# Kernel optimization log

Measured on AMD Instinct MI355X. Metric: run time of the kernel, lower is better.

The kernel has to match this reference:

```python
import jax, jax.numpy as jnp
import numpy as np

FEATURES = 8
POINTS = 3
CLASSES = 128
BATCH = 1024
TEMPERATURE = 0.1


def setup_inputs() -> dict:
    key = jax.random.key(0)
    k1, k2, k3 = jax.random.split(key, 3)
    x = jax.random.normal(k1, (BATCH, FEATURES), dtype=jnp.float32)
    beta = jax.random.uniform(k2, (FEATURES, POINTS), dtype=jnp.float32)
    classifier = jax.random.uniform(
        k3, ((POINTS + 1) ** FEATURES, CLASSES), dtype=jnp.float32)
    return {"x": x, "beta": beta, "classifier": classifier}


def reference(x, beta, classifier):
    # b: sort beta ascending per-feature, negate, cumsum, prepend a zero bin edge
    T = 1.0 / TEMPERATURE
    bneg = jnp.cumsum(-jnp.sort(beta, axis=1), axis=1)            # [F, P]
    b = jnp.concatenate(
        [jnp.zeros((beta.shape[0], 1), beta.dtype), bneg], axis=1)  # [F, P+1]
    w = jnp.arange(1, POINTS + 2, dtype=x.dtype)                  # [P+1]
    # soft one-hot binning per feature: [B, F, P+1]
    logits = (x[:, :, None] * w[None, None, :] + b[None, :, :]) * T
    hot = jax.nn.softmax(logits, axis=-1)
    # iterative outer product over features -> joint leaf histogram [B, (P+1)^F]
    B = x.shape[0]
    leaves = hot[:, 0, :]
    for f in range(1, FEATURES):  # small fixed loop over features
        leaves = (leaves[:, :, None] * hot[:, f, None, :]).reshape(B, -1)
    return leaves @ classifier  # [B, classes]
```

## Files before the change

kernel.cpp:

```cpp
#include <hip/hip_runtime.h>
#include <stdint.h>

typedef unsigned short u16;
typedef __attribute__((ext_vector_type(4))) float f32x4;
typedef __attribute__((ext_vector_type(2))) float f32x2;
typedef __attribute__((ext_vector_type(8))) short s16x8;

#define T_INV 10.0f
#define QEPS 9.5367431640625e-07f

__device__ __forceinline__ u16 f2bf(float f) {
  uint32_t u = __float_as_uint(f);
  uint32_t r = (u + 0x7FFFu + ((u >> 16) & 1u)) >> 16;
  return (u16)r;
}

__device__ __forceinline__ void gload_lds16(const void* g, void* l) {
  __builtin_amdgcn_global_load_lds(
      (const __attribute__((address_space(1))) uint32_t*)(g),
      (__attribute__((address_space(3))) uint32_t*)(l),
      16, 0, 0);
}

__global__ __launch_bounds__(256) void k_prep(
    const float* __restrict__ cls, const float* __restrict__ x,
    const float* __restrict__ beta,
    u16* __restrict__ ct, u16* __restrict__ plo, float* __restrict__ phiT)
{
  const int t = threadIdx.x;
  if (blockIdx.x < 1024) {
    __shared__ float tile[64 * 132];
    const int k0 = blockIdx.x * 64;
#pragma unroll
    for (int it = 0; it < 8; ++it) {
      int e = it * 1024 + t * 4;
      int r = e >> 7;
      int c = e & 127;
      f32x4 v = *(const f32x4*)(cls + (size_t)(k0 + r) * 128 + c);
      *(f32x4*)(tile + r * 132 + c) = v;
    }
    __syncthreads();
    const int c  = t >> 1;
    const int kh = t & 1;
    u16 vals[32];
#pragma unroll
    for (int j = 0; j < 32; ++j)
      vals[j] = f2bf(tile[(kh*32 + j) * 132 + c]);
    u16* dst = ct + ((size_t)(k0 >> 3) + kh * 4) * 1024 + c * 8;
#pragma unroll
    for (int qq = 0; qq < 4; ++qq) {
      s16x8 v;
#pragma unroll
      for (int e2 = 0; e2 < 8; ++e2) v[e2] = (short)vals[qq*8 + e2];
      *(s16x8*)(dst + (size_t)qq * 1024) = v;
    }
  } else {
    const int b = (blockIdx.x - 1024) * 64 + (t >> 2);
    const int q = t & 3;
    float hot[8][4];
#pragma unroll
    for (int f = 0; f < 8; ++f) {
      float b0 = beta[f*3+0], b1 = beta[f*3+1], b2 = beta[f*3+2];
      float s0 = fminf(b0, fminf(b1, b2));
      float s2 = fmaxf(b0, fmaxf(b1, b2));
      float s1 = b0 + b1 + b2 - s0 - s2;
      float bv1 = -s0, bv2 = -(s0 + s1), bv3 = -(s0 + s1 + s2);
      float xf = x[b*8 + f];
      float l0 = (xf * 1.0f       ) * T_INV;
      float l1 = (xf * 2.0f + bv1) * T_INV;
      float l2 = (xf * 3.0f + bv2) * T_INV;
      float l3 = (xf * 4.0f + bv3) * T_INV;
      float mm = fmaxf(fmaxf(l0, l1), fmaxf(l2, l3));
      float e0 = __expf(l0 - mm), e1 = __expf(l1 - mm);
      float e2 = __expf(l2 - mm), e3 = __expf(l3 - mm);
      float inv = 1.0f / (e0 + e1 + e2 + e3);
      hot[f][0] = e0*inv; hot[f][1] = e1*inv; hot[f][2] = e2*inv; hot[f][3] = e3*inv;
    }
    {
      float h23[16];
#pragma unroll
      for (int i2 = 0; i2 < 4; ++i2)
#pragma unroll
        for (int i3 = 0; i3 < 4; ++i3) h23[i2*4+i3] = hot[2][i2] * hot[3][i3];
      float h0q = hot[0][q];
#pragma unroll
      for (int i1 = 0; i1 < 4; ++i1) {
        float c01 = h0q * hot[1][i1];
#pragma unroll
        for (int j = 0; j < 16; ++j)
          phiT[(size_t)(q*64 + i1*16 + j) * 1024 + b] = c01 * h23[j];
      }
    }
    {
      float h67[16];
#pragma unroll
      for (int i6 = 0; i6 < 4; ++i6)
#pragma unroll
        for (int i7 = 0; i7 < 4; ++i7) h67[i6*4+i7] = hot[6][i6] * hot[7][i7];
      float h4q = hot[4][q];
      u16* dst = plo + (size_t)b*256 + q*64;
#pragma unroll
      for (int i5 = 0; i5 < 4; ++i5) {
        float c45 = h4q * hot[5][i5];
#pragma unroll
        for (int j = 0; j < 16; j += 8) {
          s16x8 v;
#pragma unroll
          for (int e = 0; e < 8; ++e) v[e] = (short)f2bf(c45 * h67[j+e]);
          *(s16x8*)(dst + i5*16 + j) = v;
        }
      }
    }
  }
}

__global__ __launch_bounds__(512, 4) void k_main(
    const u16* __restrict__ plo, const float* __restrict__ phiT,
    const u16* __restrict__ ct, u16* __restrict__ pws)
{
  __shared__ __align__(16) u16 As[32768];
  __shared__ __align__(16) u16 Bb[2][4096];

  const int wg  = blockIdx.x;
  const int xcd = wg & 7;
  const int idx = wg >> 3;
  const int hig = xcd * 8 + (idx >> 3);
  const int m   = idx & 7;

  const int t    = threadIdx.x;
  const int l    = t & 63;
  const int w    = t >> 6;
  const int lrow = l & 15;
  const int kg   = l >> 4;
  const int rbase = (w >> 2) * 64;
  const int cbase = (w & 3) * 32;

  const u16* ploM = plo + (size_t)m * 128 * 256;

#pragma unroll
  for (int i = 0; i < 8; ++i) {
    int row = t >> 2;
    int g   = ((t & 3) - ((t >> 3) & 3)) & 3;
    gload_lds16(ploM + (size_t)row * 256 + i * 32 + g * 8, &As[i * 4096 + t * 8]);
  }

  int aoff[4], boff[2];
#pragma unroll
  for (int mt = 0; mt < 4; ++mt) {
    int row = rbase + mt * 16 + lrow;
    aoff[mt] = row * 32 + (((kg + ((row >> 1) & 3)) & 3)) * 8;
  }
#pragma unroll
  for (int nt = 0; nt < 2; ++nt) {
    int c = cbase + nt * 16 + lrow;
    boff[nt] = c * 32 + (((kg + ((c >> 1) & 3)) & 3)) * 8;
  }

  const int bc = t & 127;
  const int bg = t >> 7;
  const u16* bsrc = ct + (size_t)hig * 131072 + (size_t)bc * 8
                       + (size_t)bg * 1024;
  const int sB = (bg + ((bc >> 1) & 3)) & 3;

  s16x8 bregE, bregO;
  bregE = *(const s16x8*)(bsrc + 0 * 4096);
  bregO = *(const s16x8*)(bsrc + 1 * 4096);
  *(s16x8*)(&Bb[0][bc * 32 + sB * 8]) = bregE;
  __syncthreads();

  f32x4 qprev[4];
  {
    const float* p0 = phiT + (size_t)(hig * 4) * 1024 + m * 128;
#pragma unroll
    for (int mt = 0; mt < 4; ++mt) {
      f32x4 q = *(const f32x4*)(p0 + rbase + mt * 16 + kg * 4);
#pragma unroll
      for (int r = 0; r < 4; ++r) qprev[mt][r] = fmaxf(q[r], QEPS);
    }
  }

  f32x4 acc[4][2];
#pragma unroll
  for (int i = 0; i < 4; ++i)
#pragma unroll
    for (int j = 0; j < 2; ++j) acc[i][j] = (f32x4)0.0f;

  s16x8 afrP[4];
#pragma unroll
  for (int mt = 0; mt < 4; ++mt)
    afrP[mt] = *(const s16x8*)(&As[aoff[mt]]);

#pragma unroll 1
  for (int h = 0; h < 4; ++h) {
#pragma unroll
    for (int ks = 0; ks < 8; ++ks) {
      const int tt = h * 8 + ks;
      if (h < 3 || ks < 6) {
        const u16* p = bsrc + (size_t)(tt + 2) * 4096;
        if (ks & 1) bregO = *(const s16x8*)p;
        else        bregE = *(const s16x8*)p;
      }
      s16x8 bfr[2];
#pragma unroll
      for (int nt = 0; nt < 2; ++nt)
        bfr[nt] = *(const s16x8*)(&Bb[ks & 1][boff[nt]]);
      __builtin_amdgcn_s_setprio(1);
#pragma unroll
      for (int mt = 0; mt < 4; ++mt)
#pragma unroll
        for (int nt = 0; nt < 2; ++nt)
          acc[mt][nt] = __builtin_amdgcn_mfma_f32_16x16x32_bf16(
              afrP[mt], bfr[nt], acc[mt][nt], 0, 0, 0);
      __builtin_amdgcn_s_setprio(0);
      {
        const int nks = (ks + 1) & 7;
#pragma unroll
        for (int mt = 0; mt < 4; ++mt)
          afrP[mt] = *(const s16x8*)(&As[nks * 4096 + aoff[mt]]);
      }
      if (h < 3 || ks < 7) {
        u16* d = &Bb[(ks + 1) & 1][bc * 32 + sB * 8];
        *(s16x8*)d = (ks & 1) ? bregE : bregO;
      }
      asm volatile("s_waitcnt lgkmcnt(0)" ::: "memory");
      __builtin_amdgcn_sched_barrier(0);
      __builtin_amdgcn_s_barrier();
      __builtin_amdgcn_sched_barrier(0);
    }
    if (h < 3) {
      const float* pn = phiT + (size_t)(hig * 4 + h + 1) * 1024 + m * 128;
#pragma unroll
      for (int mt = 0; mt < 4; ++mt) {
        f32x4 qn = *(const f32x4*)(pn + rbase + mt * 16 + kg * 4);
        f32x4 ratio;
#pragma unroll
        for (int r = 0; r < 4; ++r) {
          float q = fmaxf(qn[r], QEPS);
          ratio[r] = qprev[mt][r] * __builtin_amdgcn_rcpf(q);
          qprev[mt][r] = q;
        }
#pragma unroll
        for (int nt = 0; nt < 2; ++nt)
#pragma unroll
          for (int r = 0; r < 4; ++r)
            acc[mt][nt][r] *= ratio[r];
      }
    }
  }

  __syncthreads();
  {
    u16* ob = As;
#pragma unroll
    for (int mt = 0; mt < 4; ++mt)
#pragma unroll
      for (int r = 0; r < 4; ++r) {
        int row = rbase + mt * 16 + kg * 4 + r;
#pragma unroll
        for (int nt = 0; nt < 2; ++nt) {
          int col = cbase + nt * 16 + lrow;
          ob[row * 136 + col] = f2bf(acc[mt][nt][r] * qprev[mt][r]);
        }
      }
    __syncthreads();
    const int row = t >> 2;
    const int q4  = t & 3;
    const u16* srcp = ob + row * 136 + q4 * 32;
    u16* gdst = pws + ((size_t)hig * 1024 + (size_t)m * 128) * 128
                    + row * 128 + q4 * 32;
#pragma unroll
    for (int i = 0; i < 4; ++i)
      *(s16x8*)(gdst + i * 8) = *(const s16x8*)(srcp + i * 8);
  }
}

__global__ __launch_bounds__(256) void k_reduce(
    const u16* __restrict__ p, float* __restrict__ out)
{
  const int g = blockIdx.x * 256 + threadIdx.x;
  const u16* src = p + (size_t)g * 2;
  float a0 = 0.0f, a1 = 0.0f;
#pragma unroll 8
  for (int hig = 0; hig < 64; ++hig) {
    uint32_t v = *(const uint32_t*)(src + (size_t)hig * 131072);
    a0 += __uint_as_float((v & 0xFFFFu) << 16);
    a1 += __uint_as_float(v & 0xFFFF0000u);
  }
  f32x2 o; o.x = a0; o.y = a1;
  *(f32x2*)(out + (size_t)g * 2) = o;
}

extern "C" void kernel_launch(void* const* d_in, const int* in_sizes, int n_in,
                              void* d_out, int out_size, void* d_ws, size_t ws_size,
                              hipStream_t stream)
{
  const float* x    = (const float*)d_in[0];
  const float* beta = (const float*)d_in[1];
  const float* cls  = (const float*)d_in[2];
  float* out = (float*)d_out;

  char* ws = (char*)d_ws;
  u16*   ct   = (u16*)ws;
  u16*   plo  = (u16*)(ws + (16u << 20));
  float* phiT = (float*)(ws + (16u << 20) + 524288);
  u16*   pws  = (u16*)(ws + (16u << 20) + 524288 + 1048576);

  k_prep<<<1040, 256, 0, stream>>>(cls, x, beta, ct, plo, phiT);
  k_main<<<512, 512, 0, stream>>>(plo, phiT, ct, pws);
  k_reduce<<<256, 256, 0, stream>>>(pws, out);
}
```

Measured before the change: 46.72 us.

## Double k_main threads, stage B via direct-to-LDS loads with 4-deep ring

```diff
diff --git a/kernel.cpp b/kernel.cpp
--- a/kernel.cpp
+++ b/kernel.cpp
@@ -114,12 +114,12 @@
   }
 }
 
-__global__ __launch_bounds__(512, 4) void k_main(
+__global__ __launch_bounds__(1024) void k_main(
     const u16* __restrict__ plo, const float* __restrict__ phiT,
     const u16* __restrict__ ct, u16* __restrict__ pws)
 {
   __shared__ __align__(16) u16 As[32768];
-  __shared__ __align__(16) u16 Bb[2][4096];
+  __shared__ __align__(16) u16 Bb[4][4096];
 
   const int wg  = blockIdx.x;
   const int xcd = wg & 7;
@@ -132,118 +132,118 @@
   const int w    = t >> 6;
   const int lrow = l & 15;
   const int kg   = l >> 4;
-  const int rbase = (w >> 2) * 64;
+  const int rbase = (w >> 2) * 32;
   const int cbase = (w & 3) * 32;
 
   const u16* ploM = plo + (size_t)m * 128 * 256;
 
 #pragma unroll
-  for (int i = 0; i < 8; ++i) {
-    int row = t >> 2;
-    int g   = ((t & 3) - ((t >> 3) & 3)) & 3;
-    gload_lds16(ploM + (size_t)row * 256 + i * 32 + g * 8, &As[i * 4096 + t * 8]);
-  }
-
-  int aoff[4], boff[2];
-#pragma unroll
-  for (int mt = 0; mt < 4; ++mt) {
+  for (int i = 0; i < 4; ++i) {
+    int ks   = i * 2 + (t >> 9);
+    int idx2 = t & 511;
+    int row  = idx2 >> 2;
+    int g    = ((idx2 & 3) - ((row >> 1) & 3)) & 3;
+    gload_lds16(ploM + (size_t)row * 256 + ks * 32 + g * 8,
+                &As[ks * 4096 + idx2 * 8]);
+  }
+
+  const int stg  = (t < 512);
+  const int scol = (t >> 2) & 127;
+  const int sgr  = ((t & 3) - ((scol >> 1) & 3)) & 3;
+  auto stageB = [&](int kc) {
+    if (stg)
+      gload_lds16(ct + (((size_t)(hig * 128 + kc * 4 + sgr)) << 10) + scol * 8,
+                  &Bb[kc & 3][(t & 511) * 8]);
+  };
+
+  stageB(0); stageB(1); stageB(2);
+  asm volatile("s_waitcnt vmcnt(0)" ::: "memory");
+  __builtin_amdgcn_sched_barrier(0);
+  __builtin_amdgcn_s_barrier();
+  __builtin_amdgcn_sched_barrier(0);
+
+  s16x8 areg[2][8];
+#pragma unroll
+  for (int mt = 0; mt < 2; ++mt) {
     int row = rbase + mt * 16 + lrow;
-    aoff[mt] = row * 32 + (((kg + ((row >> 1) & 3)) & 3)) * 8;
-  }
+    int off = row * 32 + (((kg + ((row >> 1) & 3)) & 3)) * 8;
+#pragma unroll
+    for (int ks = 0; ks < 8; ++ks)
+      areg[mt][ks] = *(const s16x8*)(&As[ks * 4096 + off]);
+  }
+
+  int boff[2];
 #pragma unroll
   for (int nt = 0; nt < 2; ++nt) {
     int c = cbase + nt * 16 + lrow;
     boff[nt] = c * 32 + (((kg + ((c >> 1) & 3)) & 3)) * 8;
   }
 
-  const int bc = t & 127;
-  const int bg = t >> 7;
-  const u16* bsrc = ct + (size_t)hig * 131072 + (size_t)bc * 8
-                       + (size_t)bg * 1024;
-  const int sB = (bg + ((bc >> 1) & 3)) & 3;
-
-  s16x8 bregE, bregO;
-  bregE = *(const s16x8*)(bsrc + 0 * 4096);
-  bregO = *(const s16x8*)(bsrc + 1 * 4096);
-  *(s16x8*)(&Bb[0][bc * 32 + sB * 8]) = bregE;
-  __syncthreads();
-
-  f32x4 qprev[4];
+  f32x4 qprev[2];
   {
     const float* p0 = phiT + (size_t)(hig * 4) * 1024 + m * 128;
 #pragma unroll
-    for (int mt = 0; mt < 4; ++mt) {
+    for (int mt = 0; mt < 2; ++mt) {
       f32x4 q = *(const f32x4*)(p0 + rbase + mt * 16 + kg * 4);
 #pragma unroll
       for (int r = 0; r < 4; ++r) qprev[mt][r] = fmaxf(q[r], QEPS);
     }
   }
 
-  f32x4 acc[4][2];
-#pragma unroll
-  for (int i = 0; i < 4; ++i)
+  f32x4 acc[2][2];
+#pragma unroll
+  for (int i = 0; i < 2; ++i)
 #pragma unroll
     for (int j = 0; j < 2; ++j) acc[i][j] = (f32x4)0.0f;
-
-  s16x8 afrP[4];
-#pragma unroll
-  for (int mt = 0; mt < 4; ++mt)
-    afrP[mt] = *(const s16x8*)(&As[aoff[mt]]);
 
 #pragma unroll 1
   for (int h = 0; h < 4; ++h) {
 #pragma unroll
     for (int ks = 0; ks < 8; ++ks) {
-      const int tt = h * 8 + ks;
-      if (h < 3 || ks < 6) {
-        const u16* p = bsrc + (size_t)(tt + 2) * 4096;
-        if (ks & 1) bregO = *(const s16x8*)p;
-        else        bregE = *(const s16x8*)p;
-      }
+      const int kc = h * 8 + ks;
+      if (h < 3 || ks < 5) stageB(kc + 3);
       s16x8 bfr[2];
 #pragma unroll
       for (int nt = 0; nt < 2; ++nt)
-        bfr[nt] = *(const s16x8*)(&Bb[ks & 1][boff[nt]]);
+        bfr[nt] = *(const s16x8*)(&Bb[ks & 3][boff[nt]]);
       __builtin_amdgcn_s_setprio(1);
 #pragma unroll
-      for (int mt = 0; mt < 4; ++mt)
+      for (int mt = 0; mt < 2; ++mt)
 #pragma unroll
         for (int nt = 0; nt < 2; ++nt)
           acc[mt][nt] = __builtin_amdgcn_mfma_f32_16x16x32_bf16(
-              afrP[mt], bfr[nt], acc[mt][nt], 0, 0, 0);
+              areg[mt][ks], bfr[nt], acc[mt][nt], 0, 0, 0);
       __builtin_amdgcn_s_setprio(0);
-      {
-        const int nks = (ks + 1) & 7;
-#pragma unroll
-        for (int mt = 0; mt < 4; ++mt)
-          afrP[mt] = *(const s16x8*)(&As[nks * 4096 + aoff[mt]]);
-      }
-      if (h < 3 || ks < 7) {
-        u16* d = &Bb[(ks + 1) & 1][bc * 32 + sB * 8];
-        *(s16x8*)d = (ks & 1) ? bregE : bregO;
-      }
-      asm volatile("s_waitcnt lgkmcnt(0)" ::: "memory");
-      __builtin_amdgcn_sched_barrier(0);
-      __builtin_amdgcn_s_barrier();
-      __builtin_amdgcn_sched_barrier(0);
-    }
-    if (h < 3) {
-      const float* pn = phiT + (size_t)(hig * 4 + h + 1) * 1024 + m * 128;
-#pragma unroll
-      for (int mt = 0; mt < 4; ++mt) {
-        f32x4 qn = *(const f32x4*)(pn + rbase + mt * 16 + kg * 4);
-        f32x4 ratio;
-#pragma unroll
-        for (int r = 0; r < 4; ++r) {
-          float q = fmaxf(qn[r], QEPS);
-          ratio[r] = qprev[mt][r] * __builtin_amdgcn_rcpf(q);
-          qprev[mt][r] = q;
+      if (ks == 7 && h < 3) {
+        const float* pn = phiT + (size_t)(hig * 4 + h + 1) * 1024 + m * 128;
+#pragma unroll
+        for (int mt = 0; mt < 2; ++mt) {
+          f32x4 qn = *(const f32x4*)(pn + rbase + mt * 16 + kg * 4);
+          f32x4 ratio;
+#pragma unroll
+          for (int r = 0; r < 4; ++r) {
+            float q = fmaxf(qn[r], QEPS);
+            ratio[r] = qprev[mt][r] * __builtin_amdgcn_rcpf(q);
+            qprev[mt][r] = q;
+          }
+#pragma unroll
+          for (int nt = 0; nt < 2; ++nt)
+#pragma unroll
+            for (int r = 0; r < 4; ++r)
+              acc[mt][nt][r] *= ratio[r];
         }
-#pragma unroll
-        for (int nt = 0; nt < 2; ++nt)
-#pragma unroll
-          for (int r = 0; r < 4; ++r)
-            acc[mt][nt][r] *= ratio[r];
+      }
+      if (kc <= 28) {
+        asm volatile("s_waitcnt vmcnt(2)" ::: "memory");
+      } else if (kc == 29) {
+        asm volatile("s_waitcnt vmcnt(1)" ::: "memory");
+      } else if (kc == 30) {
+        asm volatile("s_waitcnt vmcnt(0)" ::: "memory");
+      }
+      if (kc < 31) {
+        __builtin_amdgcn_sched_barrier(0);
+        __builtin_amdgcn_s_barrier();
+        __builtin_amdgcn_sched_barrier(0);
       }
     }
   }
@@ -252,7 +252,7 @@
   {
     u16* ob = As;
 #pragma unroll
-    for (int mt = 0; mt < 4; ++mt)
+    for (int mt = 0; mt < 2; ++mt)
 #pragma unroll
       for (int r = 0; r < 4; ++r) {
         int row = rbase + mt * 16 + kg * 4 + r;
@@ -263,14 +263,13 @@
         }
       }
     __syncthreads();
-    const int row = t >> 2;
-    const int q4  = t & 3;
-    const u16* srcp = ob + row * 136 + q4 * 32;
-    u16* gdst = pws + ((size_t)hig * 1024 + (size_t)m * 128) * 128
-                    + row * 128 + q4 * 32;
-#pragma unroll
-    for (int i = 0; i < 4; ++i)
-      *(s16x8*)(gdst + i * 8) = *(const s16x8*)(srcp + i * 8);
+    const int row = t >> 3;
+    const int seg = t & 7;
+    const u16* srcp = ob + row * 136 + seg * 16;
+    u16* gdst = pws + ((size_t)hig * 1024 + (size_t)m * 128 + row) * 128
+                    + seg * 16;
+    *(s16x8*)(gdst)     = *(const s16x8*)(srcp);
+    *(s16x8*)(gdst + 8) = *(const s16x8*)(srcp + 8);
   }
 }
 
@@ -306,6 +305,6 @@
   u16*   pws  = (u16*)(ws + (16u << 20) + 524288 + 1048576);
 
   k_prep<<<1040, 256, 0, stream>>>(cls, x, beta, ct, plo, phiT);
-  k_main<<<512, 512, 0, stream>>>(plo, phiT, ct, pws);
+  k_main<<<512, 1024, 0, stream>>>(plo, phiT, ct, pws);
   k_reduce<<<256, 256, 0, stream>>>(pws, out);
 }
```

After: 50.62 us. 1.08x slower.

## Stage B tiles via direct global-to-LDS loads with coarser double buffering

Applied to the files above, without the earlier changes.

```diff
diff --git a/kernel.cpp b/kernel.cpp
--- a/kernel.cpp
+++ b/kernel.cpp
@@ -114,12 +114,12 @@
   }
 }
 
-__global__ __launch_bounds__(512, 4) void k_main(
+__global__ __launch_bounds__(512) void k_main(
     const u16* __restrict__ plo, const float* __restrict__ phiT,
     const u16* __restrict__ ct, u16* __restrict__ pws)
 {
   __shared__ __align__(16) u16 As[32768];
-  __shared__ __align__(16) u16 Bb[2][4096];
+  __shared__ __align__(16) u16 Bp[2][16384];
 
   const int wg  = blockIdx.x;
   const int xcd = wg & 7;
@@ -140,9 +140,20 @@
 #pragma unroll
   for (int i = 0; i < 8; ++i) {
     int row = t >> 2;
-    int g   = ((t & 3) - ((t >> 3) & 3)) & 3;
+    int g   = ((t & 3) - ((row >> 1) & 3)) & 3;
     gload_lds16(ploM + (size_t)row * 256 + i * 32 + g * 8, &As[i * 4096 + t * 8]);
   }
+
+  const int scol = t >> 2;
+  const int ssl  = t & 3;
+  const int sgr  = (ssl - ((scol >> 1) & 3)) & 3;
+  auto stageB = [&](int p, int buf) {
+#pragma unroll
+    for (int s = 0; s < 4; ++s)
+      gload_lds16(ct + (((size_t)(hig * 128 + p * 16 + s * 4 + sgr)) << 10)
+                     + scol * 8,
+                  &Bp[buf][s * 4096 + t * 8]);
+  };
 
   int aoff[4], boff[2];
 #pragma unroll
@@ -156,17 +167,11 @@
     boff[nt] = c * 32 + (((kg + ((c >> 1) & 3)) & 3)) * 8;
   }
 
-  const int bc = t & 127;
-  const int bg = t >> 7;
-  const u16* bsrc = ct + (size_t)hig * 131072 + (size_t)bc * 8
-                       + (size_t)bg * 1024;
-  const int sB = (bg + ((bc >> 1) & 3)) & 3;
-
-  s16x8 bregE, bregO;
-  bregE = *(const s16x8*)(bsrc + 0 * 4096);
-  bregO = *(const s16x8*)(bsrc + 1 * 4096);
-  *(s16x8*)(&Bb[0][bc * 32 + sB * 8]) = bregE;
-  __syncthreads();
+  stageB(0, 0);
+  asm volatile("s_waitcnt vmcnt(0)" ::: "memory");
+  __builtin_amdgcn_sched_barrier(0);
+  __builtin_amdgcn_s_barrier();
+  __builtin_amdgcn_sched_barrier(0);
 
   f32x4 qprev[4];
   {
@@ -185,50 +190,31 @@
 #pragma unroll
     for (int j = 0; j < 2; ++j) acc[i][j] = (f32x4)0.0f;
 
-  s16x8 afrP[4];
-#pragma unroll
-  for (int mt = 0; mt < 4; ++mt)
-    afrP[mt] = *(const s16x8*)(&As[aoff[mt]]);
-
 #pragma unroll 1
-  for (int h = 0; h < 4; ++h) {
-#pragma unroll
-    for (int ks = 0; ks < 8; ++ks) {
-      const int tt = h * 8 + ks;
-      if (h < 3 || ks < 6) {
-        const u16* p = bsrc + (size_t)(tt + 2) * 4096;
-        if (ks & 1) bregO = *(const s16x8*)p;
-        else        bregE = *(const s16x8*)p;
-      }
-      s16x8 bfr[2];
+  for (int p = 0; p < 8; ++p) {
+    if (p < 7) stageB(p + 1, (p + 1) & 1);
+    const u16* B  = &Bp[p & 1][0];
+    const int ksb = (p & 1) * 4;
+#pragma unroll
+    for (int s = 0; s < 4; ++s) {
+      s16x8 afr[4], bfr[2];
+#pragma unroll
+      for (int mt = 0; mt < 4; ++mt)
+        afr[mt] = *(const s16x8*)(&As[(ksb + s) * 4096 + aoff[mt]]);
 #pragma unroll
       for (int nt = 0; nt < 2; ++nt)
-        bfr[nt] = *(const s16x8*)(&Bb[ks & 1][boff[nt]]);
+        bfr[nt] = *(const s16x8*)(B + s * 4096 + boff[nt]);
       __builtin_amdgcn_s_setprio(1);
 #pragma unroll
       for (int mt = 0; mt < 4; ++mt)
 #pragma unroll
         for (int nt = 0; nt < 2; ++nt)
           acc[mt][nt] = __builtin_amdgcn_mfma_f32_16x16x32_bf16(
-              afrP[mt], bfr[nt], acc[mt][nt], 0, 0, 0);
+              afr[mt], bfr[nt], acc[mt][nt], 0, 0, 0);
       __builtin_amdgcn_s_setprio(0);
-      {
-        const int nks = (ks + 1) & 7;
-#pragma unroll
-        for (int mt = 0; mt < 4; ++mt)
-          afrP[mt] = *(const s16x8*)(&As[nks * 4096 + aoff[mt]]);
-      }
-      if (h < 3 || ks < 7) {
-        u16* d = &Bb[(ks + 1) & 1][bc * 32 + sB * 8];
-        *(s16x8*)d = (ks & 1) ? bregE : bregO;
-      }
-      asm volatile("s_waitcnt lgkmcnt(0)" ::: "memory");
-      __builtin_amdgcn_sched_barrier(0);
-      __builtin_amdgcn_s_barrier();
-      __builtin_amdgcn_sched_barrier(0);
-    }
-    if (h < 3) {
-      const float* pn = phiT + (size_t)(hig * 4 + h + 1) * 1024 + m * 128;
+    }
+    if ((p & 1) && p < 7) {
+      const float* pn = phiT + (size_t)(hig * 4 + (p >> 1) + 1) * 1024 + m * 128;
 #pragma unroll
       for (int mt = 0; mt < 4; ++mt) {
         f32x4 qn = *(const f32x4*)(pn + rbase + mt * 16 + kg * 4);
@@ -245,6 +231,12 @@
           for (int r = 0; r < 4; ++r)
             acc[mt][nt][r] *= ratio[r];
       }
+    }
+    if (p < 7) {
+      asm volatile("s_waitcnt vmcnt(0)" ::: "memory");
+      __builtin_amdgcn_sched_barrier(0);
+      __builtin_amdgcn_s_barrier();
+      __builtin_amdgcn_sched_barrier(0);
     }
   }
 
@@ -264,10 +256,10 @@
       }
     __syncthreads();
     const int row = t >> 2;
-    const int q4  = t & 3;
-    const u16* srcp = ob + row * 136 + q4 * 32;
-    u16* gdst = pws + ((size_t)hig * 1024 + (size_t)m * 128) * 128
-                    + row * 128 + q4 * 32;
+    const int seg = t & 3;
+    const u16* srcp = ob + row * 136 + seg * 32;
+    u16* gdst = pws + ((size_t)hig * 1024 + (size_t)m * 128 + row) * 128
+                    + seg * 32;
 #pragma unroll
     for (int i = 0; i < 4; ++i)
       *(s16x8*)(gdst + i * 8) = *(const s16x8*)(srcp + i * 8);
```

Result: slower. 61.32 us (+31.3%).
